# Kernel tuning notes

Measured on AMD Instinct MI355X. Metric: run time of the kernel, lower is better.

## Reference

```python
import jax, jax.numpy as jnp
import numpy as np

D_KQ = 1024

def setup_inputs() -> dict:
    key = jax.random.key(0)
    k1, k2, k3, k4, k5 = jax.random.split(key, 5)
    x = jax.random.normal(k1, (4, 2048, 1024), dtype=jnp.float32)
    attention_mask = jax.random.randint(k2, (2048, 2048), 0, 2) == 1
    q_weights = jax.random.normal(k3, (1024, 1024), dtype=jnp.float32)
    k_weights = jax.random.normal(k4, (1024, 1024), dtype=jnp.float32)
    v_weights = jax.random.normal(k5, (1024, 1024), dtype=jnp.float32)
    return {"x": x, "attention_mask": attention_mask,
            "q_weights": q_weights, "k_weights": k_weights, "v_weights": v_weights}

def reference(x, attention_mask, q_weights, k_weights, v_weights):
    # projections: [B,S,d_in] @ [d_in,d] -> [B,S,d]
    query = x @ q_weights
    key = x @ k_weights
    value = x @ v_weights
    # scores: [B,S,S]
    attn_scores = jnp.einsum('bqd,bkd->bqk', query, key)
    masked = jnp.where(attention_mask, -jnp.inf, attn_scores)
    attn_weights = jax.nn.softmax(masked / jnp.sqrt(jnp.float32(D_KQ)), axis=-1)
    return attn_weights @ value
```

## Files before the change

kernel.cpp:

```cpp
#include <hip/hip_runtime.h>
#include <math.h>

static constexpr int BATCH = 4;
static constexpr int SEQ   = 2048;
static constexpr int DIM   = 1024;

typedef __attribute__((ext_vector_type(8))) short     bf16x8;
typedef __attribute__((ext_vector_type(4))) float     f32x4;

__device__ __forceinline__ unsigned short f2b(float v) {
    unsigned int u = __float_as_uint(v);
    u = u + 0x7fffu + ((u >> 16) & 1u);
    return (unsigned short)(u >> 16);
}
__device__ __forceinline__ float b2f(unsigned short h) {
    return __uint_as_float(((unsigned int)h) << 16);
}

__global__ __launch_bounds__(256) void convert_x_kernel(
    const float* __restrict__ X, unsigned short* __restrict__ hi,
    unsigned short* __restrict__ lo)
{
    const int i = blockIdx.x * 256 + threadIdx.x;
    const float4 v = ((const float4*)X)[i];
    ushort4 h, l;
    h.x = f2b(v.x); l.x = f2b(v.x - b2f(h.x));
    h.y = f2b(v.y); l.y = f2b(v.y - b2f(h.y));
    h.z = f2b(v.z); l.z = f2b(v.z - b2f(h.z));
    h.w = f2b(v.w); l.w = f2b(v.w - b2f(h.w));
    ((ushort4*)hi)[i] = h;
    ((ushort4*)lo)[i] = l;
}

__global__ __launch_bounds__(256) void convert_wqk_kernel(
    const float* __restrict__ Wq, const float* __restrict__ Wk,
    unsigned short* __restrict__ hi, unsigned short* __restrict__ lo)
{
    const int z = blockIdx.y;
    const float* __restrict__ W = z ? Wk : Wq;
    const int i = blockIdx.x * 256 + threadIdx.x;
    const int o = z * (DIM * DIM / 4) + i;
    const float4 v = ((const float4*)W)[i];
    ushort4 h, l;
    h.x = f2b(v.x); l.x = f2b(v.x - b2f(h.x));
    h.y = f2b(v.y); l.y = f2b(v.y - b2f(h.y));
    h.z = f2b(v.z); l.z = f2b(v.z - b2f(h.z));
    h.w = f2b(v.w); l.w = f2b(v.w - b2f(h.w));
    ((ushort4*)hi)[o] = h;
    ((ushort4*)lo)[o] = l;
}

__global__ __launch_bounds__(256) void convert_wv_kernel(
    const float* __restrict__ W, unsigned short* __restrict__ WT)
{
    __shared__ float t[32][33];
    const int n0 = blockIdx.x * 32, k0 = blockIdx.y * 32;
    const int tx = threadIdx.x & 31, ty = threadIdx.x >> 5;
#pragma unroll
    for (int i = 0; i < 4; ++i)
        t[ty + i * 8][tx] = W[(size_t)(k0 + ty + i * 8) * DIM + (n0 + tx)];
    __syncthreads();
#pragma unroll
    for (int i = 0; i < 4; ++i)
        WT[(size_t)(n0 + ty + i * 8) * DIM + (k0 + tx)] = f2b(t[tx][ty + i * 8]);
}

__device__ __forceinline__ void stage_async(
    const unsigned short* __restrict__ g, int gstride, int row0, int k0,
    unsigned short* lds, int tid)
{
    const int w = tid >> 6, lane = tid & 63;
    const int c = (lane & 3) ^ ((lane >> 4) & 3);
#pragma unroll
    for (int h = 0; h < 2; ++h) {
        const int row = 32 * w + 16 * h + (lane >> 2);
        const unsigned short* src = g + (size_t)(row0 + row) * gstride + k0 + 8 * c;
        unsigned short* dst = lds + (32 * w + 16 * h) * 32;
        __builtin_amdgcn_global_load_lds(
            (const __attribute__((address_space(1))) void*)src,
            (__attribute__((address_space(3))) void*)dst, 16, 0, 0);
    }
}

__device__ __forceinline__ bf16x8 fragr(const unsigned short* lds, int row, int qsw)
{
    return *(const bf16x8*)(lds + row * 32 + qsw * 8);
}

__global__ __launch_bounds__(256) void m_gemm_kernel(
    const unsigned short* __restrict__ Whi, const unsigned short* __restrict__ Wlo,
    float* __restrict__ Mtp)
{
    __shared__ unsigned short Ah[128 * 32], Al[128 * 32];
    __shared__ unsigned short Bh[128 * 32], Bl[128 * 32];

    const int tid = threadIdx.x;
    const int w = tid >> 6, lane = tid & 63;
    const int wm = (w >> 1) * 64, wn = (w & 1) * 64;
    const int m0 = blockIdx.y * 128, n0 = blockIdx.x * 128;
    const int z = blockIdx.z;

    const unsigned short* __restrict__ Ahg = Whi + (size_t)DIM * DIM;
    const unsigned short* __restrict__ Alg = Wlo + (size_t)DIM * DIM;
    const unsigned short* __restrict__ Bhg = Whi;
    const unsigned short* __restrict__ Blg = Wlo;
    float* __restrict__ Cp = Mtp + (size_t)z * DIM * DIM;

    f32x4 acc[4][4];
#pragma unroll
    for (int i = 0; i < 4; ++i)
#pragma unroll
        for (int j = 0; j < 4; ++j) acc[i][j] = (f32x4){0.f, 0.f, 0.f, 0.f};

    const int fr = lane & 15, quad = lane >> 4;
    const int qsw = quad ^ ((fr >> 2) & 3);

    for (int k0 = z * 256; k0 < z * 256 + 256; k0 += 32) {
        stage_async(Ahg, DIM, m0, k0, Ah, tid);
        stage_async(Alg, DIM, m0, k0, Al, tid);
        stage_async(Bhg, DIM, n0, k0, Bh, tid);
        stage_async(Blg, DIM, n0, k0, Bl, tid);
        __syncthreads();

        bf16x8 ah[4], al[4];
#pragma unroll
        for (int mt = 0; mt < 4; ++mt) {
            ah[mt] = fragr(Ah, wm + mt * 16 + fr, qsw);
            al[mt] = fragr(Al, wm + mt * 16 + fr, qsw);
        }
#pragma unroll
        for (int nt = 0; nt < 4; ++nt) {
            const bf16x8 bh = fragr(Bh, wn + nt * 16 + fr, qsw);
            const bf16x8 bl = fragr(Bl, wn + nt * 16 + fr, qsw);
#pragma unroll
            for (int mt = 0; mt < 4; ++mt) {
                acc[mt][nt] = __builtin_amdgcn_mfma_f32_16x16x32_bf16(ah[mt], bh, acc[mt][nt], 0, 0, 0);
                acc[mt][nt] = __builtin_amdgcn_mfma_f32_16x16x32_bf16(ah[mt], bl, acc[mt][nt], 0, 0, 0);
                acc[mt][nt] = __builtin_amdgcn_mfma_f32_16x16x32_bf16(al[mt], bh, acc[mt][nt], 0, 0, 0);
            }
        }
        __syncthreads();
    }

    const int col = lane & 15, rq = lane >> 4;
#pragma unroll
    for (int mt = 0; mt < 4; ++mt)
#pragma unroll
        for (int nt = 0; nt < 4; ++nt)
#pragma unroll
            for (int e = 0; e < 4; ++e) {
                const int m = m0 + wm + mt * 16 + rq * 4 + e;
                const int n = n0 + wn + nt * 16 + col;
                Cp[(size_t)m * DIM + n] = acc[mt][nt][e];
            }
}

__global__ __launch_bounds__(256) void m_reduce_kernel(
    const float* __restrict__ Mtp, unsigned short* __restrict__ Mthi,
    unsigned short* __restrict__ Mtlo)
{
    const int i = blockIdx.x * 256 + threadIdx.x;
    const size_t q = (size_t)DIM * DIM / 4;
    const float4 a = ((const float4*)Mtp)[i];
    const float4 b = ((const float4*)Mtp)[i + q];
    const float4 c = ((const float4*)Mtp)[i + 2 * q];
    const float4 d = ((const float4*)Mtp)[i + 3 * q];
    const float4 v = make_float4(a.x + b.x + c.x + d.x, a.y + b.y + c.y + d.y,
                                 a.z + b.z + c.z + d.z, a.w + b.w + c.w + d.w);
    ushort4 h, l;
    h.x = f2b(v.x); l.x = f2b(v.x - b2f(h.x));
    h.y = f2b(v.y); l.y = f2b(v.y - b2f(h.y));
    h.z = f2b(v.z); l.z = f2b(v.z - b2f(h.z));
    h.w = f2b(v.w); l.w = f2b(v.w - b2f(h.w));
    ((ushort4*)Mthi)[i] = h;
    ((ushort4*)Mtlo)[i] = l;
}

__global__ __launch_bounds__(256) void yv_gemm_kernel(
    const unsigned short* __restrict__ Xhi, const unsigned short* __restrict__ Xlo,
    const unsigned short* __restrict__ Mthi, const unsigned short* __restrict__ Mtlo,
    const unsigned short* __restrict__ WvT,
    unsigned short* __restrict__ Yhi, unsigned short* __restrict__ Ylo,
    unsigned short* __restrict__ Vt)
{
    __shared__ unsigned short Ah[128 * 32], Al[128 * 32];
    __shared__ unsigned short Bh[128 * 32], Bl[128 * 32];

    const int tid = threadIdx.x;
    const int w = tid >> 6, lane = tid & 63;
    const int wm = (w >> 1) * 64, wn = (w & 1) * 64;
    const int m0 = blockIdx.y * 128, n0 = blockIdx.x * 128;
    const int z = blockIdx.z;
    const bool full = (z == 0);

    const unsigned short* __restrict__ Bhg = full ? Mthi : WvT;
    const unsigned short* __restrict__ Blg = Mtlo;

    f32x4 acc[4][4];
#pragma unroll
    for (int i = 0; i < 4; ++i)
#pragma unroll
        for (int j = 0; j < 4; ++j) acc[i][j] = (f32x4){0.f, 0.f, 0.f, 0.f};

    const int fr = lane & 15, quad = lane >> 4;
    const int qsw = quad ^ ((fr >> 2) & 3);

    for (int k0 = 0; k0 < DIM; k0 += 32) {
        stage_async(Xhi, DIM, m0, k0, Ah, tid);
        stage_async(Bhg, DIM, n0, k0, Bh, tid);
        if (full) {
            stage_async(Xlo, DIM, m0, k0, Al, tid);
            stage_async(Blg, DIM, n0, k0, Bl, tid);
        }
        __syncthreads();

        bf16x8 ah[4], al[4];
#pragma unroll
        for (int mt = 0; mt < 4; ++mt)
            ah[mt] = fragr(Ah, wm + mt * 16 + fr, qsw);
        if (full) {
#pragma unroll
            for (int mt = 0; mt < 4; ++mt)
                al[mt] = fragr(Al, wm + mt * 16 + fr, qsw);
        }
#pragma unroll
        for (int nt = 0; nt < 4; ++nt) {
            const bf16x8 bh = fragr(Bh, wn + nt * 16 + fr, qsw);
#pragma unroll
            for (int mt = 0; mt < 4; ++mt)
                acc[mt][nt] = __builtin_amdgcn_mfma_f32_16x16x32_bf16(ah[mt], bh, acc[mt][nt], 0, 0, 0);
            if (full) {
                const bf16x8 bl = fragr(Bl, wn + nt * 16 + fr, qsw);
#pragma unroll
                for (int mt = 0; mt < 4; ++mt) {
                    acc[mt][nt] = __builtin_amdgcn_mfma_f32_16x16x32_bf16(ah[mt], bl, acc[mt][nt], 0, 0, 0);
                    acc[mt][nt] = __builtin_amdgcn_mfma_f32_16x16x32_bf16(al[mt], bh, acc[mt][nt], 0, 0, 0);
                }
            }
        }
        __syncthreads();
    }

    const int col = lane & 15, rq = lane >> 4;
    if (full) {
#pragma unroll
        for (int mt = 0; mt < 4; ++mt)
#pragma unroll
            for (int nt = 0; nt < 4; ++nt)
#pragma unroll
                for (int e = 0; e < 4; ++e) {
                    const int m = m0 + wm + mt * 16 + rq * 4 + e;
                    const int n = n0 + wn + nt * 16 + col;
                    const float v = acc[mt][nt][e];
                    const unsigned short h = f2b(v);
                    Yhi[(size_t)m * DIM + n] = h;
                    Ylo[(size_t)m * DIM + n] = f2b(v - b2f(h));
                }
    } else {
#pragma unroll
        for (int mt = 0; mt < 4; ++mt)
#pragma unroll
            for (int nt = 0; nt < 4; ++nt) {
                const int m = m0 + wm + mt * 16 + rq * 4;
                const int bb = m >> 11, s = m & (SEQ - 1);
                const int n = n0 + wn + nt * 16 + col;
                ushort4 pk;
                pk.x = f2b(acc[mt][nt][0]);
                pk.y = f2b(acc[mt][nt][1]);
                pk.z = f2b(acc[mt][nt][2]);
                pk.w = f2b(acc[mt][nt][3]);
                *(ushort4*)(Vt + (size_t)bb * DIM * SEQ + (size_t)n * SEQ + s) = pk;
            }
    }
}

__global__ __launch_bounds__(256) void s_gemm_kernel(
    const unsigned short* __restrict__ Yhi, const unsigned short* __restrict__ Ylo,
    const unsigned short* __restrict__ Xhi, const unsigned short* __restrict__ Xlo,
    const int* __restrict__ mask, float* __restrict__ Sc)
{
    __shared__ unsigned short Ah[128 * 32], Al[128 * 32];
    __shared__ unsigned short Bh[128 * 32], Bl[128 * 32];

    const int tid = threadIdx.x;
    const int w = tid >> 6, lane = tid & 63;
    const int wm = (w >> 1) * 64, wn = (w & 1) * 64;
    const int m0 = blockIdx.y * 128, n0 = blockIdx.x * 128;
    const int b = blockIdx.z;

    const unsigned short* __restrict__ Ahg = Yhi + (size_t)b * SEQ * DIM;
    const unsigned short* __restrict__ Alg = Ylo + (size_t)b * SEQ * DIM;
    const unsigned short* __restrict__ Bhg = Xhi + (size_t)b * SEQ * DIM;
    const unsigned short* __restrict__ Blg = Xlo + (size_t)b * SEQ * DIM;
    float* __restrict__ Sb = Sc + (size_t)b * SEQ * SEQ;

    f32x4 acc[4][4];
#pragma unroll
    for (int i = 0; i < 4; ++i)
#pragma unroll
        for (int j = 0; j < 4; ++j) acc[i][j] = (f32x4){0.f, 0.f, 0.f, 0.f};

    const int fr = lane & 15, quad = lane >> 4;
    const int qsw = quad ^ ((fr >> 2) & 3);

    for (int k0 = 0; k0 < DIM; k0 += 32) {
        stage_async(Ahg, DIM, m0, k0, Ah, tid);
        stage_async(Alg, DIM, m0, k0, Al, tid);
        stage_async(Bhg, DIM, n0, k0, Bh, tid);
        stage_async(Blg, DIM, n0, k0, Bl, tid);
        __syncthreads();

        bf16x8 ah[4], al[4];
#pragma unroll
        for (int mt = 0; mt < 4; ++mt) {
            ah[mt] = fragr(Ah, wm + mt * 16 + fr, qsw);
            al[mt] = fragr(Al, wm + mt * 16 + fr, qsw);
        }
#pragma unroll
        for (int nt = 0; nt < 4; ++nt) {
            const bf16x8 bh = fragr(Bh, wn + nt * 16 + fr, qsw);
            const bf16x8 bl = fragr(Bl, wn + nt * 16 + fr, qsw);
#pragma unroll
            for (int mt = 0; mt < 4; ++mt) {
                acc[mt][nt] = __builtin_amdgcn_mfma_f32_16x16x32_bf16(ah[mt], bh, acc[mt][nt], 0, 0, 0);
                acc[mt][nt] = __builtin_amdgcn_mfma_f32_16x16x32_bf16(ah[mt], bl, acc[mt][nt], 0, 0, 0);
                acc[mt][nt] = __builtin_amdgcn_mfma_f32_16x16x32_bf16(al[mt], bh, acc[mt][nt], 0, 0, 0);
            }
        }
        __syncthreads();
    }

    const int col = lane & 15, rq = lane >> 4;
#pragma unroll
    for (int mt = 0; mt < 4; ++mt)
#pragma unroll
        for (int nt = 0; nt < 4; ++nt)
#pragma unroll
            for (int e = 0; e < 4; ++e) {
                const int m = m0 + wm + mt * 16 + rq * 4 + e;
                const int n = n0 + wn + nt * 16 + col;
                const float v = acc[mt][nt][e] * 0.03125f;
                Sb[(size_t)m * SEQ + n] = mask[(size_t)m * SEQ + n] ? -INFINITY : v;
            }
}

__global__ __launch_bounds__(256) void softmax_kernel(float* __restrict__ Sc)
{
    const int r = blockIdx.x;
    float* __restrict__ row = Sc + (size_t)r * SEQ;

    const int tid  = threadIdx.x;
    const int lane = tid & 63;
    const int wid  = tid >> 6;

    float x[8];
    float mx = -INFINITY;
#pragma unroll
    for (int j = 0; j < 8; ++j) {
        x[j] = row[tid + j * 256];
        mx = fmaxf(mx, x[j]);
    }
    __shared__ float redm[4];
#pragma unroll
    for (int off = 32; off > 0; off >>= 1)
        mx = fmaxf(mx, __shfl_down(mx, off, 64));
    if (lane == 0) redm[wid] = mx;
    __syncthreads();
    mx = fmaxf(fmaxf(redm[0], redm[1]), fmaxf(redm[2], redm[3]));

    float sum = 0.f;
#pragma unroll
    for (int j = 0; j < 8; ++j) {
        const float e = __expf(x[j] - mx);
        x[j] = e;
        sum += e;
    }
    __shared__ float reds[4];
#pragma unroll
    for (int off = 32; off > 0; off >>= 1)
        sum += __shfl_down(sum, off, 64);
    if (lane == 0) reds[wid] = sum;
    __syncthreads();
    sum = (reds[0] + reds[1]) + (reds[2] + reds[3]);

    const float inv = 1.0f / sum;
    unsigned short* __restrict__ prow = (unsigned short*)row;
#pragma unroll
    for (int j = 0; j < 8; ++j)
        prow[tid + j * 256] = f2b(x[j] * inv);
}

__global__ __launch_bounds__(256) void pv_mfma_kernel(
    const unsigned short* __restrict__ P, const unsigned short* __restrict__ Vt,
    float* __restrict__ O)
{
    __shared__ unsigned short As[2][128 * 32], Bs[2][128 * 32];

    const int tid = threadIdx.x;
    const int w = tid >> 6, lane = tid & 63;
    const int wm = (w >> 1) * 64, wn = (w & 1) * 64;
    const int m0 = blockIdx.y * 128, n0 = blockIdx.x * 128;
    const int b = blockIdx.z;

    const unsigned short* __restrict__ Ag = P + (size_t)b * SEQ * (2 * SEQ);
    const unsigned short* __restrict__ Bg = Vt + (size_t)b * DIM * SEQ;
    float* __restrict__ Ob = O + (size_t)b * SEQ * DIM;

    f32x4 acc[4][4];
#pragma unroll
    for (int i = 0; i < 4; ++i)
#pragma unroll
        for (int j = 0; j < 4; ++j) acc[i][j] = (f32x4){0.f, 0.f, 0.f, 0.f};

    const int fr = lane & 15, quad = lane >> 4;
    const int qsw = quad ^ ((fr >> 2) & 3);

    for (int k0 = 0; k0 < SEQ; k0 += 64) {
        stage_async(Ag, 2 * SEQ, m0, k0,      As[0], tid);
        stage_async(Ag, 2 * SEQ, m0, k0 + 32, As[1], tid);
        stage_async(Bg, SEQ,     n0, k0,      Bs[0], tid);
        stage_async(Bg, SEQ,     n0, k0 + 32, Bs[1], tid);
        __syncthreads();

#pragma unroll
        for (int s = 0; s < 2; ++s) {
            bf16x8 af[4];
#pragma unroll
            for (int mt = 0; mt < 4; ++mt)
                af[mt] = fragr(As[s], wm + mt * 16 + fr, qsw);
#pragma unroll
            for (int nt = 0; nt < 4; ++nt) {
                const bf16x8 bfg = fragr(Bs[s], wn + nt * 16 + fr, qsw);
#pragma unroll
                for (int mt = 0; mt < 4; ++mt)
                    acc[mt][nt] = __builtin_amdgcn_mfma_f32_16x16x32_bf16(af[mt], bfg, acc[mt][nt], 0, 0, 0);
            }
        }
        __syncthreads();
    }

    const int col = lane & 15, rq = lane >> 4;
#pragma unroll
    for (int mt = 0; mt < 4; ++mt)
#pragma unroll
        for (int nt = 0; nt < 4; ++nt)
#pragma unroll
            for (int e = 0; e < 4; ++e) {
                const int m = m0 + wm + mt * 16 + rq * 4 + e;
                const int n = n0 + wn + nt * 16 + col;
                Ob[(size_t)m * DIM + n] = acc[mt][nt][e];
            }
}

extern "C" void kernel_launch(void* const* d_in, const int* in_sizes, int n_in,
                              void* d_out, int out_size, void* d_ws, size_t ws_size,
                              hipStream_t stream)
{
    const float* x    = (const float*)d_in[0];
    const int*   mask = (const int*)d_in[1];
    const float* wq   = (const float*)d_in[2];
    const float* wk   = (const float*)d_in[3];
    const float* wv   = (const float*)d_in[4];
    float* out = (float*)d_out;

    const size_t NQ = (size_t)BATCH * SEQ * DIM;
    const size_t NM = (size_t)DIM * DIM;
    unsigned short* Xhi  = (unsigned short*)d_ws;
    unsigned short* Xlo  = Xhi + NQ;
    unsigned short* Yhi  = Xlo + NQ;
    unsigned short* Ylo  = Yhi + NQ;
    unsigned short* Vt   = Ylo + NQ;
    unsigned short* Mthi = Vt + NQ;
    unsigned short* Mtlo = Mthi + NM;
    float* Sc = (float*)(Mtlo + NM);

    unsigned short* Whi = (unsigned short*)Sc;
    unsigned short* Wlo = Whi + 2 * NM;
    unsigned short* WvT = Wlo + 2 * NM;
    float* Mtp = (float*)(WvT + NM);

    convert_x_kernel<<<dim3(NQ / 4 / 256), 256, 0, stream>>>(x, Xhi, Xlo);
    convert_wqk_kernel<<<dim3(NM / 4 / 256, 2), 256, 0, stream>>>(wq, wk, Whi, Wlo);
    convert_wv_kernel<<<dim3(32, 32), 256, 0, stream>>>(wv, WvT);
    m_gemm_kernel<<<dim3(8, 8, 4), 256, 0, stream>>>(Whi, Wlo, Mtp);
    m_reduce_kernel<<<dim3(NM / 4 / 256), 256, 0, stream>>>(Mtp, Mthi, Mtlo);
    yv_gemm_kernel<<<dim3(DIM / 128, (BATCH * SEQ) / 128, 2), 256, 0, stream>>>(
        Xhi, Xlo, Mthi, Mtlo, WvT, Yhi, Ylo, Vt);
    s_gemm_kernel<<<dim3(SEQ / 128, SEQ / 128, BATCH), 256, 0, stream>>>(
        Yhi, Ylo, Xhi, Xlo, mask, Sc);
    softmax_kernel<<<dim3(BATCH * SEQ), 256, 0, stream>>>(Sc);
    pv_mfma_kernel<<<dim3(DIM / 128, SEQ / 128, BATCH), 256, 0, stream>>>(
        (const unsigned short*)Sc, Vt, out);
}
```

Before: 391.8 us.

## Use 256x256 double-buffered S GEMM tile with 8-wave interleaved prefetch

Replaces the 128x128 single-buffered score GEMM with a 256x256 tile computed by 512 threads. Operands are staged into 128 KB of double-buffered dynamic LDS, and the next k-slice's global loads are issued between MFMA phases. Each phase is raised with s_setprio to overlap memory with compute and to increase operand reuse per loaded byte. The cost is more LDS and registers per block, so only one block fits per CU. The grid shrinks to 256 blocks, which leaves little room for load balancing.

Measured after the change: 386.5 us. About the same (-1.4%).

```diff
diff --git a/kernel.cpp b/kernel.cpp
--- a/kernel.cpp
+++ b/kernel.cpp
@@ -274,18 +274,17 @@
     }
 }
 
-__global__ __launch_bounds__(256) void s_gemm_kernel(
+__global__ __launch_bounds__(512, 2) void s_gemm256_kernel(
     const unsigned short* __restrict__ Yhi, const unsigned short* __restrict__ Ylo,
     const unsigned short* __restrict__ Xhi, const unsigned short* __restrict__ Xlo,
     const int* __restrict__ mask, float* __restrict__ Sc)
 {
-    __shared__ unsigned short Ah[128 * 32], Al[128 * 32];
-    __shared__ unsigned short Bh[128 * 32], Bl[128 * 32];
+    extern __shared__ unsigned short smem[];
 
     const int tid = threadIdx.x;
     const int w = tid >> 6, lane = tid & 63;
-    const int wm = (w >> 1) * 64, wn = (w & 1) * 64;
-    const int m0 = blockIdx.y * 128, n0 = blockIdx.x * 128;
+    const int wm = (w >> 2) * 128, wn = (w & 3) * 64;
+    const int m0 = blockIdx.y * 256, n0 = blockIdx.x * 256;
     const int b = blockIdx.z;
 
     const unsigned short* __restrict__ Ahg = Yhi + (size_t)b * SEQ * DIM;
@@ -294,45 +293,122 @@
     const unsigned short* __restrict__ Blg = Xlo + (size_t)b * SEQ * DIM;
     float* __restrict__ Sb = Sc + (size_t)b * SEQ * SEQ;
 
-    f32x4 acc[4][4];
-#pragma unroll
-    for (int i = 0; i < 4; ++i)
+    f32x4 acc[8][4];
+#pragma unroll
+    for (int i = 0; i < 8; ++i)
 #pragma unroll
         for (int j = 0; j < 4; ++j) acc[i][j] = (f32x4){0.f, 0.f, 0.f, 0.f};
 
     const int fr = lane & 15, quad = lane >> 4;
     const int qsw = quad ^ ((fr >> 2) & 3);
 
-    for (int k0 = 0; k0 < DIM; k0 += 32) {
-        stage_async(Ahg, DIM, m0, k0, Ah, tid);
-        stage_async(Alg, DIM, m0, k0, Al, tid);
-        stage_async(Bhg, DIM, n0, k0, Bh, tid);
-        stage_async(Blg, DIM, n0, k0, Bl, tid);
-        __syncthreads();
-
-        bf16x8 ah[4], al[4];
+    stage_async(Ahg, DIM, m0, 0, smem + 0,     tid);
+    stage_async(Alg, DIM, m0, 0, smem + 8192,  tid);
+    stage_async(Bhg, DIM, n0, 0, smem + 16384, tid);
+    stage_async(Blg, DIM, n0, 0, smem + 24576, tid);
+    asm volatile("s_waitcnt vmcnt(0)" ::: "memory");
+    __builtin_amdgcn_s_barrier();
+
+    for (int it = 0; it < DIM / 32; ++it) {
+        const int cur = (it & 1) * 32768;
+        const int nxt = cur ^ 32768;
+        const unsigned short* Ah = smem + cur;
+        const unsigned short* Al = smem + cur + 8192;
+        const unsigned short* Bh = smem + cur + 16384;
+        const unsigned short* Bl = smem + cur + 24576;
+        const int k1 = it * 32 + 32;
+        const bool pf = (it < DIM / 32 - 1);
+
+        bf16x8 ah[4], al[4], bh[2], bl[2];
+
+        if (pf) {
+            stage_async(Ahg, DIM, m0, k1, smem + nxt,        tid);
+            stage_async(Alg, DIM, m0, k1, smem + nxt + 8192, tid);
+        }
 #pragma unroll
         for (int mt = 0; mt < 4; ++mt) {
             ah[mt] = fragr(Ah, wm + mt * 16 + fr, qsw);
             al[mt] = fragr(Al, wm + mt * 16 + fr, qsw);
         }
 #pragma unroll
-        for (int nt = 0; nt < 4; ++nt) {
-            const bf16x8 bh = fragr(Bh, wn + nt * 16 + fr, qsw);
-            const bf16x8 bl = fragr(Bl, wn + nt * 16 + fr, qsw);
+        for (int j = 0; j < 2; ++j) {
+            bh[j] = fragr(Bh, wn + j * 16 + fr, qsw);
+            bl[j] = fragr(Bl, wn + j * 16 + fr, qsw);
+        }
+        __builtin_amdgcn_s_barrier();
+        __builtin_amdgcn_s_setprio(1);
+#pragma unroll
+        for (int j = 0; j < 2; ++j)
 #pragma unroll
             for (int mt = 0; mt < 4; ++mt) {
-                acc[mt][nt] = __builtin_amdgcn_mfma_f32_16x16x32_bf16(ah[mt], bh, acc[mt][nt], 0, 0, 0);
-                acc[mt][nt] = __builtin_amdgcn_mfma_f32_16x16x32_bf16(ah[mt], bl, acc[mt][nt], 0, 0, 0);
-                acc[mt][nt] = __builtin_amdgcn_mfma_f32_16x16x32_bf16(al[mt], bh, acc[mt][nt], 0, 0, 0);
-            }
-        }
-        __syncthreads();
+                acc[mt][j] = __builtin_amdgcn_mfma_f32_16x16x32_bf16(ah[mt], bh[j], acc[mt][j], 0, 0, 0);
+                acc[mt][j] = __builtin_amdgcn_mfma_f32_16x16x32_bf16(ah[mt], bl[j], acc[mt][j], 0, 0, 0);
+                acc[mt][j] = __builtin_amdgcn_mfma_f32_16x16x32_bf16(al[mt], bh[j], acc[mt][j], 0, 0, 0);
+            }
+        __builtin_amdgcn_s_setprio(0);
+
+        if (pf) {
+            stage_async(Bhg, DIM, n0, k1, smem + nxt + 16384, tid);
+            stage_async(Blg, DIM, n0, k1, smem + nxt + 24576, tid);
+        }
+#pragma unroll
+        for (int j = 0; j < 2; ++j) {
+            bh[j] = fragr(Bh, wn + 32 + j * 16 + fr, qsw);
+            bl[j] = fragr(Bl, wn + 32 + j * 16 + fr, qsw);
+        }
+        __builtin_amdgcn_s_barrier();
+        __builtin_amdgcn_s_setprio(1);
+#pragma unroll
+        for (int j = 0; j < 2; ++j)
+#pragma unroll
+            for (int mt = 0; mt < 4; ++mt) {
+                acc[mt][2 + j] = __builtin_amdgcn_mfma_f32_16x16x32_bf16(ah[mt], bh[j], acc[mt][2 + j], 0, 0, 0);
+                acc[mt][2 + j] = __builtin_amdgcn_mfma_f32_16x16x32_bf16(ah[mt], bl[j], acc[mt][2 + j], 0, 0, 0);
+                acc[mt][2 + j] = __builtin_amdgcn_mfma_f32_16x16x32_bf16(al[mt], bh[j], acc[mt][2 + j], 0, 0, 0);
+            }
+        __builtin_amdgcn_s_setprio(0);
+
+#pragma unroll
+        for (int mt = 0; mt < 4; ++mt) {
+            ah[mt] = fragr(Ah, wm + 64 + mt * 16 + fr, qsw);
+            al[mt] = fragr(Al, wm + 64 + mt * 16 + fr, qsw);
+        }
+        __builtin_amdgcn_s_barrier();
+        __builtin_amdgcn_s_setprio(1);
+#pragma unroll
+        for (int j = 0; j < 2; ++j)
+#pragma unroll
+            for (int mt = 0; mt < 4; ++mt) {
+                acc[4 + mt][2 + j] = __builtin_amdgcn_mfma_f32_16x16x32_bf16(ah[mt], bh[j], acc[4 + mt][2 + j], 0, 0, 0);
+                acc[4 + mt][2 + j] = __builtin_amdgcn_mfma_f32_16x16x32_bf16(ah[mt], bl[j], acc[4 + mt][2 + j], 0, 0, 0);
+                acc[4 + mt][2 + j] = __builtin_amdgcn_mfma_f32_16x16x32_bf16(al[mt], bh[j], acc[4 + mt][2 + j], 0, 0, 0);
+            }
+        __builtin_amdgcn_s_setprio(0);
+
+#pragma unroll
+        for (int j = 0; j < 2; ++j) {
+            bh[j] = fragr(Bh, wn + j * 16 + fr, qsw);
+            bl[j] = fragr(Bl, wn + j * 16 + fr, qsw);
+        }
+        __builtin_amdgcn_s_barrier();
+        __builtin_amdgcn_s_setprio(1);
+#pragma unroll
+        for (int j = 0; j < 2; ++j)
+#pragma unroll
+            for (int mt = 0; mt < 4; ++mt) {
+                acc[4 + mt][j] = __builtin_amdgcn_mfma_f32_16x16x32_bf16(ah[mt], bh[j], acc[4 + mt][j], 0, 0, 0);
+                acc[4 + mt][j] = __builtin_amdgcn_mfma_f32_16x16x32_bf16(ah[mt], bl[j], acc[4 + mt][j], 0, 0, 0);
+                acc[4 + mt][j] = __builtin_amdgcn_mfma_f32_16x16x32_bf16(al[mt], bh[j], acc[4 + mt][j], 0, 0, 0);
+            }
+        __builtin_amdgcn_s_setprio(0);
+
+        asm volatile("s_waitcnt vmcnt(0)" ::: "memory");
+        __builtin_amdgcn_s_barrier();
     }
 
     const int col = lane & 15, rq = lane >> 4;
 #pragma unroll
-    for (int mt = 0; mt < 4; ++mt)
+    for (int mt = 0; mt < 8; ++mt)
 #pragma unroll
         for (int nt = 0; nt < 4; ++nt)
 #pragma unroll
@@ -479,6 +555,14 @@
     unsigned short* WvT = Wlo + 2 * NM;
     float* Mtp = (float*)(WvT + NM);
 
+    static bool lds_attr_set = false;
+    if (!lds_attr_set) {
+        (void)hipFuncSetAttribute((const void*)s_gemm256_kernel,
+                                  hipFuncAttributeMaxDynamicSharedMemorySize,
+                                  131072);
+        lds_attr_set = true;
+    }
+
     convert_x_kernel<<<dim3(NQ / 4 / 256), 256, 0, stream>>>(x, Xhi, Xlo);
     convert_wqk_kernel<<<dim3(NM / 4 / 256, 2), 256, 0, stream>>>(wq, wk, Whi, Wlo);
     convert_wv_kernel<<<dim3(32, 32), 256, 0, stream>>>(wv, WvT);
@@ -486,7 +570,7 @@
     m_reduce_kernel<<<dim3(NM / 4 / 256), 256, 0, stream>>>(Mtp, Mthi, Mtlo);
     yv_gemm_kernel<<<dim3(DIM / 128, (BATCH * SEQ) / 128, 2), 256, 0, stream>>>(
         Xhi, Xlo, Mthi, Mtlo, WvT, Yhi, Ylo, Vt);
-    s_gemm_kernel<<<dim3(SEQ / 128, SEQ / 128, BATCH), 256, 0, stream>>>(
+    s_gemm256_kernel<<<dim3(SEQ / 256, SEQ / 256, BATCH), 512, 131072, stream>>>(
         Yhi, Ylo, Xhi, Xlo, mask, Sc);
     softmax_kernel<<<dim3(BATCH * SEQ), 256, 0, stream>>>(Sc);
     pv_mfma_kernel<<<dim3(DIM / 128, SEQ / 128, BATCH), 256, 0, stream>>>(
```
